# Kernel optimization log

Hardware: AMD Instinct MI355X
Metric: run time of the kernel (lower is better)

The kernel has to match this reference:

```python
import jax, jax.numpy as jnp
import numpy as np

B, S, D = 2, 2048, 1024
H, KV, HD = 16, 4, 64
E, TOPK, F = 8, 2, 2048
EPS = 1e-5
THETA = 10000.0


def setup_inputs() -> dict:
    key = jax.random.key(0)
    ks = jax.random.split(key, 12)
    sc = 0.02
    x = jax.random.normal(ks[0], (B, S, D), jnp.float32)
    # real RoPE tables
    inv = 1.0 / (THETA ** (np.arange(0, HD, 2, dtype=np.float32) / HD))
    t = np.arange(S, dtype=np.float32)
    f = np.outer(t, inv)  # [S, HD/2]
    freqs_cos = jnp.asarray(np.cos(f), jnp.float32)
    freqs_sin = jnp.asarray(np.sin(f), jnp.float32)
    return {
        "x": x,
        "freqs_cos": freqs_cos,
        "freqs_sin": freqs_sin,
        "attn_norm_w": jnp.ones((D,), jnp.float32),
        "ffn_norm_w": jnp.ones((D,), jnp.float32),
        "wq": jax.random.normal(ks[1], (D, H * HD), jnp.float32) * sc,
        "wk": jax.random.normal(ks[2], (D, KV * HD), jnp.float32) * sc,
        "wv": jax.random.normal(ks[3], (D, KV * HD), jnp.float32) * sc,
        "wo": jax.random.normal(ks[4], (H * HD, D), jnp.float32) * sc,
        "gate_w": jax.random.normal(ks[5], (D, E), jnp.float32) * sc,
        "w1": jax.random.normal(ks[6], (E, D, F), jnp.float32) * sc,
        "w2": jax.random.normal(ks[7], (E, F, D), jnp.float32) * sc,
        "w3": jax.random.normal(ks[8], (E, D, F), jnp.float32) * sc,
    }


def rmsnorm(x, w):
    return x * jax.lax.rsqrt(jnp.mean(x * x, axis=-1, keepdims=True) + EPS) * w


def apply_rope(xq, cos, sin):
    # xq: [B,S,h,HD]; cos/sin: [S, HD/2]
    xr, xi = xq[..., 0::2], xq[..., 1::2]
    c = cos[None, :, None, :]
    s = sin[None, :, None, :]
    out = jnp.stack([xr * c - xi * s, xr * s + xi * c], axis=-1)
    return out.reshape(xq.shape)


def attention(xn, freqs_cos, freqs_sin, wq, wk, wv, wo):
    q = (xn @ wq).reshape(B, S, H, HD)
    k = (xn @ wk).reshape(B, S, KV, HD)
    v = (xn @ wv).reshape(B, S, KV, HD)
    q = apply_rope(q, freqs_cos, freqs_sin)
    k = apply_rope(k, freqs_cos, freqs_sin)
    n_rep = H // KV
    k = jnp.repeat(k, n_rep, axis=2)  # [B,S,H,HD]
    v = jnp.repeat(v, n_rep, axis=2)
    scores = jnp.einsum("bqhd,bkhd->bhqk", q, k) / jnp.sqrt(jnp.float32(HD))
    causal = jnp.tril(jnp.ones((S, S), bool))
    scores = jnp.where(causal[None, None], scores, jnp.finfo(scores.dtype).min)
    probs = jax.nn.softmax(scores, axis=-1)
    out = jnp.einsum("bhqk,bkhd->bqhd", probs, v).reshape(B, S, H * HD)
    return out @ wo


def sparse_moe(hn, gate_w, w1, w2, w3):
    xf = hn.reshape(-1, D)  # [T, D]
    probs = jax.nn.softmax(xf @ gate_w, axis=-1)  # [T, E]
    topv, topi = jax.lax.top_k(probs, TOPK)
    topv = topv / jnp.sum(topv, axis=-1, keepdims=True)
    # dense [T, E] routing weights (0 for non-selected experts)
    wdense = jnp.sum(jax.nn.one_hot(topi, E, dtype=xf.dtype) * topv[..., None], axis=1)
    h1 = jax.nn.silu(jnp.einsum("td,edf->etf", xf, w1))
    h3 = jnp.einsum("td,edf->etf", xf, w3)
    y = jnp.einsum("etf,efd->etd", h1 * h3, w2)
    out = jnp.einsum("te,etd->td", wdense, y)
    return out.reshape(B, S, D)


def reference(x, freqs_cos, freqs_sin, attn_norm_w, ffn_norm_w,
              wq, wk, wv, wo, gate_w, w1, w2, w3):
    h = x + attention(rmsnorm(x, attn_norm_w), freqs_cos, freqs_sin, wq, wk, wv, wo)
    out = h + sparse_moe(rmsnorm(h, ffn_norm_w), gate_w, w1, w2, w3)
    return out
```

## Files before the change

### kernel.cpp

```cpp
#include <hip/hip_runtime.h>
#include <stdint.h>

typedef unsigned short u16;
typedef unsigned int u32;
typedef __attribute__((ext_vector_type(8))) short short8;
typedef __attribute__((ext_vector_type(8))) u16 us8;
typedef __attribute__((ext_vector_type(4))) u16 us4;
typedef __attribute__((ext_vector_type(4))) float f32x4;

constexpr int NB = 2;
constexpr int SEQ = 2048;
constexpr int DIM = 1024;
constexpr int NH = 16;
constexpr int HD = 64;
constexpr int NE = 8;
constexpr int FF = 2048;
constexpr int TOK = NB * SEQ;
constexpr int NQKV = 1536;
constexpr int NPAIR = TOK * 2;
constexpr float REPS = 1e-5f;

__device__ __forceinline__ u16 f2bf(float x) {
  union { float f; u32 u; } v; v.f = x;
  u32 r = v.u + 0x7fffu + ((v.u >> 16) & 1u);
  return (u16)(r >> 16);
}
__device__ __forceinline__ float bf2f(u16 h) {
  union { u32 u; float f; } v; v.u = ((u32)h) << 16;
  return v.f;
}

__device__ __forceinline__ void gl_lds16(const u16* g, u16* l) {
  __builtin_amdgcn_global_load_lds(
      (const __attribute__((address_space(1))) void*)g,
      (__attribute__((address_space(3))) void*)l, 16, 0, 0);
}

template <bool SPLIT>
__global__ __launch_bounds__(256) void tcvt_k(const float* __restrict__ src,
                                              u16* __restrict__ dhi,
                                              u16* __restrict__ dlo,
                                              int K, int N) {
  int z = blockIdx.z;
  src += (size_t)z * K * N;
  dhi += (size_t)z * K * N;
  if (SPLIT) dlo += (size_t)z * K * N;
  int n0 = blockIdx.x * 64, k0 = blockIdx.y * 64;
  __shared__ float tile[64][65];
  int t = threadIdx.x;
  int kk = t >> 4, nn4 = (t & 15) * 4;
#pragma unroll
  for (int i = 0; i < 4; i++) {
    int k = kk + i * 16;
    const float* p = src + (size_t)(k0 + k) * N + n0 + nn4;
    float4 v = *(const float4*)p;
    tile[nn4 + 0][k] = v.x;
    tile[nn4 + 1][k] = v.y;
    tile[nn4 + 2][k] = v.z;
    tile[nn4 + 3][k] = v.w;
  }
  __syncthreads();
  int nn = t >> 4, k4 = (t & 15) * 4;
#pragma unroll
  for (int i = 0; i < 4; i++) {
    int n = nn + i * 16;
    us4 hi, lo;
#pragma unroll
    for (int j = 0; j < 4; j++) {
      float f = tile[n][k4 + j];
      u16 h = f2bf(f);
      hi[j] = h;
      if (SPLIT) lo[j] = f2bf(f - bf2f(h));
    }
    *(us4*)(dhi + (size_t)(n0 + n) * K + k0 + k4) = hi;
    if (SPLIT) *(us4*)(dlo + (size_t)(n0 + n) * K + k0 + k4) = lo;
  }
}

template <bool SPLIT>
__global__ __launch_bounds__(256) void rmsnorm_k(const float* __restrict__ x,
                                                 const float* __restrict__ w,
                                                 u16* __restrict__ ohi,
                                                 u16* __restrict__ olo) {
  int row = blockIdx.x, t = threadIdx.x;
  float4 v = *(const float4*)(x + (size_t)row * DIM + t * 4);
  float ss = v.x * v.x + v.y * v.y + v.z * v.z + v.w * v.w;
#pragma unroll
  for (int m = 1; m < 64; m <<= 1) ss += __shfl_xor(ss, m);
  __shared__ float red[4];
  if ((t & 63) == 0) red[t >> 6] = ss;
  __syncthreads();
  float rstd = rsqrtf((red[0] + red[1] + red[2] + red[3]) * (1.0f / DIM) + REPS);
  float4 wv = *(const float4*)(w + t * 4);
  float os[4] = {v.x * rstd * wv.x, v.y * rstd * wv.y, v.z * rstd * wv.z,
                 v.w * rstd * wv.w};
  us4 hi, lo;
#pragma unroll
  for (int j = 0; j < 4; j++) {
    u16 h = f2bf(os[j]);
    hi[j] = h;
    if (SPLIT) lo[j] = f2bf(os[j] - bf2f(h));
  }
  *(us4*)(ohi + (size_t)row * DIM + t * 4) = hi;
  if (SPLIT) *(us4*)(olo + (size_t)row * DIM + t * 4) = lo;
}

template <int EPI, bool SPLIT, bool DUAL, bool PERSIST, bool GATHER, int NXL,
          int NT, int BN>
__global__ __launch_bounds__(256, 2) void gemm_k(
    const u16* __restrict__ Ah, const u16* __restrict__ Al,
    const u16* __restrict__ Bh, const u16* __restrict__ Bl,
    const u16* __restrict__ Bd, int N, int ldc,
    float* __restrict__ Cf, u16* __restrict__ Cb, float* __restrict__ C2,
    const float* __restrict__ resid, const int* __restrict__ cnt,
    const int* __restrict__ pids, const float* __restrict__ pw,
    const int* __restrict__ plan) {
  constexpr int K = NT * 64;
  constexpr int WCOL = BN / 2;
  constexpr int FN = BN / 32;

  int tid = threadIdx.x, lane = tid & 63, wid = tid >> 6;
  int wm = wid >> 1, wn = wid & 1;
  int rr = lane & 15, g = lane >> 4;

  __shared__ u16 sAh[128 * 64];
  __shared__ u16 sAl[SPLIT ? 128 * 64 : 16];
  __shared__ u16 sBh[BN * 64];
  __shared__ u16 sBl[SPLIT ? BN * 64 : 16];
  __shared__ u16 sB1[DUAL ? BN * 64 : 16];
  __shared__ int spid[PERSIST ? 128 : 8];
  __shared__ int srow[GATHER ? 128 : 8];

  int pl[9];
  int items;
  if (PERSIST) {
#pragma unroll
    for (int e = 0; e < 9; e++) pl[e] = plan[e];
    items = pl[8] << NXL;
  } else {
    items = 1;
  }

  int it0, itstep;
  if (PERSIST) {
    int nb = gridDim.x;
    it0 = ((nb & 7) == 0) ? ((blockIdx.x & 7) * (nb >> 3) + (blockIdx.x >> 3))
                          : blockIdx.x;
    itstep = nb;
  } else {
    it0 = 0;
    itstep = 1;
  }
  for (int w = it0; w < items; w += itstep) {
    int m0, n0, z, yt, cntz;
    if (PERSIST) {
      int wy = w >> NXL;
      int x = w & ((1 << NXL) - 1);
      z = 0;
#pragma unroll
      for (int e = 1; e < 8; e++) z += (wy >= pl[e]) ? 1 : 0;
      yt = wy - pl[z];
      m0 = wy * 128;
      n0 = x * BN;
      cntz = cnt[z];
      __syncthreads();
      if (tid < 128) {
        int i = yt * 128 + tid;
        if (i > cntz - 1) i = cntz - 1;
        int p = pids[z * NPAIR + i];
        spid[tid] = p;
        if (GATHER) srow[tid] = p >> 1;
      }
      __syncthreads();
    } else {
      int gx = gridDim.x;
      int nb = gx * gridDim.y;
      int lin = blockIdx.y * gx + blockIdx.x;
      int v = ((nb & 7) == 0) ? ((lin & 7) * (nb >> 3) + (lin >> 3)) : lin;
      m0 = (v / gx) * 128;
      n0 = (v % gx) * BN;
      z = 0;
      yt = 0;
      cntz = 1 << 30;
    }

    const u16* Bhz = Bh + (size_t)z * N * K;
    const u16* Blz = SPLIT ? Bl + (size_t)z * N * K : nullptr;
    const u16* Bdz = DUAL ? Bd + (size_t)z * N * K : nullptr;

    const u16 *agh[4], *agl[SPLIT ? 4 : 1];
    int aoff[4];
#pragma unroll
    for (int i = 0; i < 4; i++) {
      int cid = tid + i * 256;
      int r = cid >> 3, c = cid & 7;
      int gr = GATHER ? srow[r] : (m0 + r);
      int sc = c ^ (r & 7);
      agh[i] = Ah + (size_t)gr * K + sc * 8;
      if (SPLIT) agl[i] = Al + (size_t)gr * K + sc * 8;
      aoff[i] = r * 64 + c * 8;
    }
    const u16 *bgh[FN], *bgl[SPLIT ? FN : 1], *bg1[DUAL ? FN : 1];
    int boff[FN];
#pragma unroll
    for (int i = 0; i < FN; i++) {
      int cid = tid + i * 256;
      int r = cid >> 3, c = cid & 7;
      int sc = c ^ (r & 7);
      size_t gr = (size_t)(n0 + r) * K + sc * 8;
      bgh[i] = Bhz + gr;
      if (SPLIT) bgl[i] = Blz + gr;
      if (DUAL) bg1[i] = Bdz + gr;
      boff[i] = r * 64 + c * 8;
    }

    f32x4 zv = {0.f, 0.f, 0.f, 0.f};
    f32x4 acc[4][FN];
    f32x4 acc1[DUAL ? 4 : 1][DUAL ? FN : 1];
#pragma unroll
    for (int a = 0; a < 4; a++)
#pragma unroll
      for (int b = 0; b < FN; b++) {
        acc[a][b] = zv;
        if (DUAL) acc1[a][b] = zv;
      }

    for (int t = 0; t < NT; t++) {
      int k0 = t * 64;
      __syncthreads();
#pragma unroll
      for (int i = 0; i < 4; i++) {
        gl_lds16(agh[i] + k0, sAh + aoff[i]);
        if (SPLIT) gl_lds16(agl[i] + k0, sAl + aoff[i]);
      }
#pragma unroll
      for (int i = 0; i < FN; i++) {
        gl_lds16(bgh[i] + k0, sBh + boff[i]);
        if (SPLIT) gl_lds16(bgl[i] + k0, sBl + boff[i]);
        if (DUAL) gl_lds16(bg1[i] + k0, sB1 + boff[i]);
      }
      __syncthreads();

#pragma unroll
      for (int kc = 0; kc < 2; kc++) {
        short8 a_h[4], a_l[SPLIT ? 4 : 1], b_h[FN], b_l[SPLIT ? FN : 1],
            b1f[DUAL ? FN : 1];
#pragma unroll
        for (int f = 0; f < 4; f++) {
          int ra = wm * 64 + f * 16 + rr;
          int off = ra * 64 + (((kc * 4 + g) ^ (ra & 7)) * 8);
          a_h[f] = *(const short8*)&sAh[off];
          if (SPLIT) a_l[f] = *(const short8*)&sAl[off];
        }
#pragma unroll
        for (int f = 0; f < FN; f++) {
          int rb = wn * WCOL + f * 16 + rr;
          int off = rb * 64 + (((kc * 4 + g) ^ (rb & 7)) * 8);
          b_h[f] = *(const short8*)&sBh[off];
          if (SPLIT) b_l[f] = *(const short8*)&sBl[off];
          if (DUAL) b1f[f] = *(const short8*)&sB1[off];
        }
#pragma unroll
        for (int fm = 0; fm < 4; fm++)
#pragma unroll
          for (int fn = 0; fn < FN; fn++) {
            acc[fm][fn] = __builtin_amdgcn_mfma_f32_16x16x32_bf16(
                a_h[fm], b_h[fn], acc[fm][fn], 0, 0, 0);
            if (SPLIT) {
              acc[fm][fn] = __builtin_amdgcn_mfma_f32_16x16x32_bf16(
                  a_h[fm], b_l[fn], acc[fm][fn], 0, 0, 0);
              acc[fm][fn] = __builtin_amdgcn_mfma_f32_16x16x32_bf16(
                  a_l[fm], b_h[fn], acc[fm][fn], 0, 0, 0);
            }
            if (DUAL)
              acc1[fm][fn] = __builtin_amdgcn_mfma_f32_16x16x32_bf16(
                  a_h[fm], b1f[fn], acc1[fm][fn], 0, 0, 0);
          }
      }
    }

#pragma unroll
    for (int fm = 0; fm < 4; fm++)
#pragma unroll
      for (int fn = 0; fn < FN; fn++)
#pragma unroll
        for (int rg = 0; rg < 4; rg++) {
          int rl = wm * 64 + fm * 16 + g * 4 + rg;
          int col = n0 + wn * WCOL + fn * 16 + rr;
          float v = acc[fm][fn][rg];
          if (EPI == 0) {
            Cf[(size_t)(m0 + rl) * ldc + col] = v;
          } else if (EPI == 1) {
            size_t idx = (size_t)(m0 + rl) * ldc + col;
            float r2 = v + resid[idx];
            Cf[idx] = r2;
            C2[idx] = r2;
          } else if (EPI == 2) {
            float gg = v / (1.0f + __expf(-v));
            float o = gg * acc1[fm][fn][rg];
            Cb[(size_t)(m0 + rl) * ldc + col] = f2bf(o);
          } else {
            int i = yt * 128 + rl;
            if (i < cntz) {
              int p = spid[rl];
              atomicAdd(&Cf[(size_t)(p >> 1) * ldc + col], pw[p] * v);
            }
          }
        }
  }
}

__global__ __launch_bounds__(256) void rope_k(float* __restrict__ qkv,
                                              const float* __restrict__ fc,
                                              const float* __restrict__ fs) {
  int idx = blockIdx.x * 256 + threadIdx.x;
  int i = idx & 31;
  int hh = (idx >> 5) % 20;
  int t = idx / 640;
  if (t >= TOK) return;
  int s = t & (SEQ - 1);
  int base = (hh < 16) ? (hh * 64) : (1024 + (hh - 16) * 64);
  float c = fc[s * 32 + i], sn = fs[s * 32 + i];
  float* p = qkv + (size_t)t * NQKV + base + 2 * i;
  float xr = p[0], xi = p[1];
  p[0] = xr * c - xi * sn;
  p[1] = xr * sn + xi * c;
}

__global__ __launch_bounds__(256) void cvtkv_k(const float* __restrict__ qkv,
                                               u16* __restrict__ Kh,
                                               u16* __restrict__ Kl,
                                               u16* __restrict__ Vh,
                                               u16* __restrict__ Vl) {
  int kvt = blockIdx.x;
  int kvh = blockIdx.y;
  int b = blockIdx.z;
  int t = threadIdx.x;
  __shared__ float vt[64][65];
  size_t tile = ((size_t)((b * 4 + kvh) * 32 + kvt)) * 4096;
  int r = t >> 2, c4 = t & 3;
  {
    const float* kp = qkv + ((size_t)(b * SEQ + kvt * 64 + r)) * NQKV + 1024 +
                      kvh * 64 + c4 * 16;
    float ff[16];
#pragma unroll
    for (int q = 0; q < 4; q++) {
      float4 f = *(const float4*)(kp + q * 4);
      ff[q * 4 + 0] = f.x; ff[q * 4 + 1] = f.y;
      ff[q * 4 + 2] = f.z; ff[q * 4 + 3] = f.w;
    }
#pragma unroll
    for (int half = 0; half < 2; half++) {
      int c = c4 * 2 + half;
      us8 hi, lo;
#pragma unroll
      for (int j = 0; j < 8; j++) {
        float f = ff[half * 8 + j];
        u16 h = f2bf(f);
        hi[j] = h;
        lo[j] = f2bf(f - bf2f(h));
      }
      int off = r * 64 + ((c ^ (r & 7)) * 8);
      *(us8*)(Kh + tile + off) = hi;
      *(us8*)(Kl + tile + off) = lo;
    }
  }
  {
    const float* vp = qkv + ((size_t)(b * SEQ + kvt * 64 + r)) * NQKV + 1280 +
                      kvh * 64 + c4 * 16;
#pragma unroll
    for (int q = 0; q < 4; q++) {
      float4 f = *(const float4*)(vp + q * 4);
      vt[r][c4 * 16 + q * 4 + 0] = f.x;
      vt[r][c4 * 16 + q * 4 + 1] = f.y;
      vt[r][c4 * 16 + q * 4 + 2] = f.z;
      vt[r][c4 * 16 + q * 4 + 3] = f.w;
    }
  }
  __syncthreads();
  {
    int d = t >> 2, g4 = t & 3;
    float ff[16];
#pragma unroll
    for (int j = 0; j < 16; j++) ff[j] = vt[g4 * 16 + j][d];
#pragma unroll
    for (int half = 0; half < 2; half++) {
      int c = g4 * 2 + half;
      us8 hi, lo;
#pragma unroll
      for (int j = 0; j < 8; j++) {
        float f = ff[half * 8 + j];
        u16 h = f2bf(f);
        hi[j] = h;
        lo[j] = f2bf(f - bf2f(h));
      }
      int off = d * 64 + ((c ^ (d & 7)) * 8);
      *(us8*)(Vh + tile + off) = hi;
      *(us8*)(Vl + tile + off) = lo;
    }
  }
}

__global__ __launch_bounds__(256, 2) void flash_k(
    const float* __restrict__ qkv, const u16* __restrict__ Kg,
    const u16* __restrict__ Klg, const u16* __restrict__ Vg,
    const u16* __restrict__ Vlg, u16* __restrict__ ah, u16* __restrict__ al) {
  int pi = blockIdx.x;
  int h = blockIdx.y;
  int b = blockIdx.z;
  int qt[2] = {31 - pi, pi};
  int kvh = h >> 2;
  int tid = threadIdx.x, lane = tid & 63, wid = tid >> 6;
  int rr = lane & 15, g = lane >> 4;

  __shared__ u16 sKh[4096], sKl[4096], sVh[4096], sVl[4096];
  __shared__ u32 sP[4][1024];

  f32x4 zv = {0.f, 0.f, 0.f, 0.f};
  short8 aqh[2][2], aql[2][2];
#pragma unroll
  for (int u = 0; u < 2; u++) {
    int qrow = qt[u] * 64 + wid * 16 + rr;
    const float* qp =
        qkv + ((size_t)(b * SEQ + qrow)) * NQKV + h * 64 + g * 8;
#pragma unroll
    for (int kc = 0; kc < 2; kc++) {
      float4 f0 = *(const float4*)(qp + kc * 32);
      float4 f1 = *(const float4*)(qp + kc * 32 + 4);
      float ff[8] = {f0.x, f0.y, f0.z, f0.w, f1.x, f1.y, f1.z, f1.w};
#pragma unroll
      for (int j = 0; j < 8; j++) {
        u16 hi = f2bf(ff[j]);
        aqh[u][kc][j] = (short)hi;
        aql[u][kc][j] = (short)f2bf(ff[j] - bf2f(hi));
      }
    }
  }

  f32x4 o[2][4];
  float m_r[2][4], l_r[2][4];
#pragma unroll
  for (int u = 0; u < 2; u++)
#pragma unroll
    for (int i = 0; i < 4; i++) {
      o[u][i] = zv;
      m_r[u][i] = -3.0e38f;
      l_r[u][i] = 0.f;
    }

  size_t tb = ((size_t)(b * 4 + kvh) * 32) * 4096;
  int so = tid * 16;
  us8 rKh[2], rKl[2], rVh[2], rVl[2];
  {
    size_t go = tb + so;
    rKh[0] = *(const us8*)(Kg + go);  rKh[1] = *(const us8*)(Kg + go + 8);
    rKl[0] = *(const us8*)(Klg + go); rKl[1] = *(const us8*)(Klg + go + 8);
    rVh[0] = *(const us8*)(Vg + go);  rVh[1] = *(const us8*)(Vg + go + 8);
    rVl[0] = *(const us8*)(Vlg + go); rVl[1] = *(const us8*)(Vlg + go + 8);
  }

  int nt = qt[0];
  for (int kvt = 0; kvt <= nt; kvt++) {
    __syncthreads();
    *(us8*)&sKh[so] = rKh[0]; *(us8*)&sKh[so + 8] = rKh[1];
    *(us8*)&sKl[so] = rKl[0]; *(us8*)&sKl[so + 8] = rKl[1];
    *(us8*)&sVh[so] = rVh[0]; *(us8*)&sVh[so + 8] = rVh[1];
    *(us8*)&sVl[so] = rVl[0]; *(us8*)&sVl[so + 8] = rVl[1];
    if (kvt < nt) {
      size_t go = tb + (size_t)(kvt + 1) * 4096 + so;
      rKh[0] = *(const us8*)(Kg + go);  rKh[1] = *(const us8*)(Kg + go + 8);
      rKl[0] = *(const us8*)(Klg + go); rKl[1] = *(const us8*)(Klg + go + 8);
      rVh[0] = *(const us8*)(Vg + go);  rVh[1] = *(const us8*)(Vg + go + 8);
      rVl[0] = *(const us8*)(Vlg + go); rVl[1] = *(const us8*)(Vlg + go + 8);
    }
    __syncthreads();

#pragma unroll
    for (int u = 0; u < 2; u++) {
      if (!(u == 1 && kvt > qt[1])) {
        float pv[4][4];
#pragma unroll
        for (int c16 = 0; c16 < 4; c16++) {
          int rk = c16 * 16 + rr;
          f32x4 sacc = zv;
#pragma unroll
          for (int kc = 0; kc < 2; kc++) {
            int sw = rk * 64 + (((kc * 4 + g) ^ (rk & 7)) * 8);
            short8 bh = *(const short8*)&sKh[sw];
            short8 bl = *(const short8*)&sKl[sw];
            sacc = __builtin_amdgcn_mfma_f32_16x16x32_bf16(aqh[u][kc], bh,
                                                           sacc, 0, 0, 0);
            sacc = __builtin_amdgcn_mfma_f32_16x16x32_bf16(aqh[u][kc], bl,
                                                           sacc, 0, 0, 0);
            sacc = __builtin_amdgcn_mfma_f32_16x16x32_bf16(aql[u][kc], bh,
                                                           sacc, 0, 0, 0);
          }
          bool diag = (kvt == qt[u]);
#pragma unroll
          for (int rg = 0; rg < 4; rg++) {
            float val = sacc[rg] * 0.125f;
            if (diag) {
              int kv_l = c16 * 16 + rr;
              int q_l = wid * 16 + g * 4 + rg;
              if (kv_l > q_l) val = -3.0e38f;
            }
            pv[c16][rg] = val;
          }
        }
        float pm[4];
#pragma unroll
        for (int rg = 0; rg < 4; rg++)
          pm[rg] = fmaxf(fmaxf(pv[0][rg], pv[1][rg]),
                         fmaxf(pv[2][rg], pv[3][rg]));
#pragma unroll
        for (int m = 1; m < 16; m <<= 1)
#pragma unroll
          for (int rg = 0; rg < 4; rg++)
            pm[rg] = fmaxf(pm[rg], __shfl_xor(pm[rg], m));
        float scl[4];
#pragma unroll
        for (int rg = 0; rg < 4; rg++) {
          float mn = fmaxf(m_r[u][rg], pm[rg]);
          scl[rg] = __expf(m_r[u][rg] - mn);
          m_r[u][rg] = mn;
        }
#pragma unroll
        for (int c16 = 0; c16 < 4; c16++)
#pragma unroll
          for (int rg = 0; rg < 4; rg++)
            pv[c16][rg] = __expf(pv[c16][rg] - m_r[u][rg]);
        float rsum[4];
#pragma unroll
        for (int rg = 0; rg < 4; rg++)
          rsum[rg] = pv[0][rg] + pv[1][rg] + pv[2][rg] + pv[3][rg];
#pragma unroll
        for (int m = 1; m < 16; m <<= 1)
#pragma unroll
          for (int rg = 0; rg < 4; rg++) rsum[rg] += __shfl_xor(rsum[rg], m);
#pragma unroll
        for (int rg = 0; rg < 4; rg++)
          l_r[u][rg] = l_r[u][rg] * scl[rg] + rsum[rg];
#pragma unroll
        for (int d16 = 0; d16 < 4; d16++)
#pragma unroll
          for (int rg = 0; rg < 4; rg++) o[u][d16][rg] *= scl[rg];

#pragma unroll
        for (int c16 = 0; c16 < 4; c16++)
#pragma unroll
          for (int rg = 0; rg < 4; rg++) {
            int ql = g * 4 + rg;
            int kvl = c16 * 16 + rr;
            u16 hi = f2bf(pv[c16][rg]);
            u16 lo = f2bf(pv[c16][rg] - bf2f(hi));
            sP[wid][ql * 64 + (kvl ^ (((ql >> 2) & 3) << 4))] =
                ((u32)lo << 16) | (u32)hi;
          }
        short8 pah[2], pal[2];
#pragma unroll
        for (int kc = 0; kc < 2; kc++) {
          int xb = (kc * 32 + g * 8) ^ (((rr >> 2) & 3) << 4);
          const u32* pp = &sP[wid][rr * 64 + xb];
#pragma unroll
          for (int j = 0; j < 8; j++) {
            u32 w = pp[j];
            pah[kc][j] = (short)(w & 0xffffu);
            pal[kc][j] = (short)(w >> 16);
          }
        }
#pragma unroll
        for (int d16 = 0; d16 < 4; d16++) {
          int rv = d16 * 16 + rr;
#pragma unroll
          for (int kc = 0; kc < 2; kc++) {
            int sw = rv * 64 + (((kc * 4 + g) ^ (rv & 7)) * 8);
            short8 vh = *(const short8*)&sVh[sw];
            short8 vl = *(const short8*)&sVl[sw];
            o[u][d16] = __builtin_amdgcn_mfma_f32_16x16x32_bf16(
                pah[kc], vh, o[u][d16], 0, 0, 0);
            o[u][d16] = __builtin_amdgcn_mfma_f32_16x16x32_bf16(
                pah[kc], vl, o[u][d16], 0, 0, 0);
            o[u][d16] = __builtin_amdgcn_mfma_f32_16x16x32_bf16(
                pal[kc], vh, o[u][d16], 0, 0, 0);
          }
        }
      }
    }
  }

#pragma unroll
  for (int u = 0; u < 2; u++)
#pragma unroll
    for (int rg = 0; rg < 4; rg++) {
      float inv = 1.0f / l_r[u][rg];
      int qr = qt[u] * 64 + wid * 16 + g * 4 + rg;
      size_t obase = (size_t)(b * SEQ + qr) * 1024 + h * 64;
#pragma unroll
      for (int d16 = 0; d16 < 4; d16++) {
        float v = o[u][d16][rg] * inv;
        u16 hi = f2bf(v);
        ah[obase + d16 * 16 + rr] = hi;
        al[obase + d16 * 16 + rr] = f2bf(v - bf2f(hi));
      }
    }
}

__global__ __launch_bounds__(256) void route_k(const float* __restrict__ h,
                                               const float* __restrict__ wffn,
                                               const float* __restrict__ gw,
                                               int* __restrict__ cnt,
                                               int* __restrict__ pids,
                                               float* __restrict__ pw) {
  int t = blockIdx.x, tid = threadIdx.x;
  float4 v = *(const float4*)(h + (size_t)t * DIM + tid * 4);
  float ss = v.x * v.x + v.y * v.y + v.z * v.z + v.w * v.w;
#pragma unroll
  for (int m = 1; m < 64; m <<= 1) ss += __shfl_xor(ss, m);
  __shared__ float red[4];
  if ((tid & 63) == 0) red[tid >> 6] = ss;
  __syncthreads();
  float rstd = rsqrtf((red[0] + red[1] + red[2] + red[3]) * (1.0f / DIM) + REPS);
  float4 wv = *(const float4*)(wffn + tid * 4);
  float xn[4] = {v.x * rstd * wv.x, v.y * rstd * wv.y, v.z * rstd * wv.z,
                 v.w * rstd * wv.w};
  float pl[8] = {0, 0, 0, 0, 0, 0, 0, 0};
#pragma unroll
  for (int j = 0; j < 4; j++) {
    const float* gp = gw + (size_t)(tid * 4 + j) * 8;
    float4 g0 = *(const float4*)gp;
    float4 g1 = *(const float4*)(gp + 4);
    pl[0] += xn[j] * g0.x; pl[1] += xn[j] * g0.y;
    pl[2] += xn[j] * g0.z; pl[3] += xn[j] * g0.w;
    pl[4] += xn[j] * g1.x; pl[5] += xn[j] * g1.y;
    pl[6] += xn[j] * g1.z; pl[7] += xn[j] * g1.w;
  }
#pragma unroll
  for (int e = 0; e < 8; e++)
#pragma unroll
    for (int m = 1; m < 64; m <<= 1) pl[e] += __shfl_xor(pl[e], m);
  __shared__ float lred[4][8];
  if ((tid & 63) == 0)
#pragma unroll
    for (int e = 0; e < 8; e++) lred[tid >> 6][e] = pl[e];
  __syncthreads();
  if (tid == 0) {
    float lg[8];
#pragma unroll
    for (int e = 0; e < 8; e++)
      lg[e] = lred[0][e] + lred[1][e] + lred[2][e] + lred[3][e];
    int e1 = 0;
    float l1 = lg[0];
#pragma unroll
    for (int e = 1; e < 8; e++)
      if (lg[e] > l1) { l1 = lg[e]; e1 = e; }
    int e2 = -1;
    float l2 = -3.0e38f;
#pragma unroll
    for (int e = 0; e < 8; e++)
      if (e != e1 && lg[e] > l2) { l2 = lg[e]; e2 = e; }
    float w1 = 1.0f / (1.0f + expf(l2 - l1));
    float w2 = 1.0f / (1.0f + expf(l1 - l2));
    int p0 = atomicAdd(&cnt[e1], 1);
    pids[e1 * NPAIR + p0] = t * 2;
    pw[t * 2] = w1;
    int p1 = atomicAdd(&cnt[e2], 1);
    pids[e2 * NPAIR + p1] = t * 2 + 1;
    pw[t * 2 + 1] = w2;
  }
}

__global__ void zero_k(int* cnt) {
  if (threadIdx.x < 8) cnt[threadIdx.x] = 0;
}

__global__ void plan_k(const int* __restrict__ cnt, int* __restrict__ plan) {
  if (threadIdx.x == 0) {
    int acc = 0;
    for (int e = 0; e < 8; e++) {
      plan[e] = acc;
      acc += (cnt[e] + 127) >> 7;
    }
    plan[8] = acc;
  }
}

extern "C" void kernel_launch(void* const* d_in, const int* in_sizes, int n_in,
                              void* d_out, int out_size, void* d_ws,
                              size_t ws_size, hipStream_t stream) {
  (void)in_sizes; (void)n_in; (void)out_size; (void)ws_size;
  const float* x = (const float*)d_in[0];
  const float* fc = (const float*)d_in[1];
  const float* fs = (const float*)d_in[2];
  const float* anw = (const float*)d_in[3];
  const float* fnw = (const float*)d_in[4];
  const float* wq = (const float*)d_in[5];
  const float* wk = (const float*)d_in[6];
  const float* wv = (const float*)d_in[7];
  const float* wo = (const float*)d_in[8];
  const float* gw = (const float*)d_in[9];
  const float* w1 = (const float*)d_in[10];
  const float* w2 = (const float*)d_in[11];
  const float* w3 = (const float*)d_in[12];
  float* outf = (float*)d_out;

  char* ws = (char*)d_ws;
  size_t off = 0;
  auto alloc = [&](size_t bytes) {
    void* p = ws + off;
    off += (bytes + 255) & ~(size_t)255;
    return p;
  };
  u16* xnh = (u16*)alloc((size_t)TOK * DIM * 2);
  u16* xnl = (u16*)alloc((size_t)TOK * DIM * 2);
  float* qkvf = (float*)alloc((size_t)TOK * NQKV * 4);
  u16* h13 = xnh;
  u16* wqkvT_h = (u16*)alloc((size_t)NQKV * DIM * 2);
  u16* wqkvT_l = (u16*)alloc((size_t)NQKV * DIM * 2);
  u16* woT_h = (u16*)alloc((size_t)DIM * DIM * 2);
  u16* woT_l = (u16*)alloc((size_t)DIM * DIM * 2);
  u16* w1T = (u16*)alloc((size_t)NE * FF * DIM * 2);
  u16* w3T = (u16*)alloc((size_t)NE * FF * DIM * 2);
  u16* w2T = (u16*)alloc((size_t)NE * DIM * FF * 2);
  u16* attnh = (u16*)alloc((size_t)TOK * DIM * 2);
  u16* attnl = (u16*)alloc((size_t)TOK * DIM * 2);
  float* hbuf = (float*)alloc((size_t)TOK * DIM * 4);
  u16* hn = (u16*)alloc((size_t)TOK * DIM * 2);
  int* cnt = (int*)alloc(64);
  int* plan = (int*)alloc(64);
  int* pids = (int*)alloc((size_t)NE * NPAIR * 4);
  float* pwbuf = (float*)alloc((size_t)NPAIR * 4);
  u16* Ksw_h = (u16*)alloc((size_t)NB * 4 * SEQ * 64 * 2);
  u16* Ksw_l = (u16*)alloc((size_t)NB * 4 * SEQ * 64 * 2);
  u16* Vsw_h = (u16*)alloc((size_t)NB * 4 * SEQ * 64 * 2);
  u16* Vsw_l = (u16*)alloc((size_t)NB * 4 * SEQ * 64 * 2);

  dim3 blk(256);
  hipLaunchKernelGGL((tcvt_k<true>), dim3(16, 16, 1), blk, 0, stream, wq,
                     wqkvT_h, wqkvT_l, 1024, 1024);
  hipLaunchKernelGGL((tcvt_k<true>), dim3(4, 16, 1), blk, 0, stream, wk,
                     wqkvT_h + 1024 * 1024, wqkvT_l + 1024 * 1024, 1024, 256);
  hipLaunchKernelGGL((tcvt_k<true>), dim3(4, 16, 1), blk, 0, stream, wv,
                     wqkvT_h + 1280 * 1024, wqkvT_l + 1280 * 1024, 1024, 256);
  hipLaunchKernelGGL((tcvt_k<true>), dim3(16, 16, 1), blk, 0, stream, wo, woT_h,
                     woT_l, 1024, 1024);
  hipLaunchKernelGGL((tcvt_k<false>), dim3(32, 16, 8), blk, 0, stream, w1, w1T,
                     (u16*)nullptr, 1024, 2048);
  hipLaunchKernelGGL((tcvt_k<false>), dim3(32, 16, 8), blk, 0, stream, w3, w3T,
                     (u16*)nullptr, 1024, 2048);
  hipLaunchKernelGGL((tcvt_k<false>), dim3(16, 32, 8), blk, 0, stream, w2, w2T,
                     (u16*)nullptr, 2048, 1024);
  hipLaunchKernelGGL((rmsnorm_k<true>), dim3(TOK), blk, 0, stream, x, anw, xnh,
                     xnl);
  hipLaunchKernelGGL((gemm_k<0, true, false, false, false, 0, 16, 64>),
                     dim3(NQKV / 64, TOK / 128, 1), blk, 0, stream, xnh, xnl,
                     wqkvT_h, wqkvT_l, (const u16*)nullptr, NQKV, NQKV, qkvf,
                     (u16*)nullptr, (float*)nullptr, (const float*)nullptr,
                     (const int*)nullptr, (const int*)nullptr,
                     (const float*)nullptr, (const int*)nullptr);
  hipLaunchKernelGGL(rope_k, dim3((TOK * 20 * 32) / 256), blk, 0, stream, qkvf,
                     fc, fs);
  hipLaunchKernelGGL(cvtkv_k, dim3(SEQ / 64, 4, NB), blk, 0, stream, qkvf,
                     Ksw_h, Ksw_l, Vsw_h, Vsw_l);
  hipLaunchKernelGGL(flash_k, dim3(16, NH, NB), blk, 0, stream, qkvf, Ksw_h,
                     Ksw_l, Vsw_h, Vsw_l, attnh, attnl);
  hipLaunchKernelGGL((gemm_k<1, true, false, false, false, 0, 16, 64>),
                     dim3(DIM / 64, TOK / 128, 1), blk, 0, stream, attnh, attnl,
                     woT_h, woT_l, (const u16*)nullptr, DIM, DIM, hbuf,
                     (u16*)nullptr, outf, x, (const int*)nullptr,
                     (const int*)nullptr, (const float*)nullptr,
                     (const int*)nullptr);
  hipLaunchKernelGGL((rmsnorm_k<false>), dim3(TOK), blk, 0, stream, hbuf, fnw,
                     hn, (u16*)nullptr);
  hipLaunchKernelGGL(zero_k, dim3(1), dim3(64), 0, stream, cnt);
  hipLaunchKernelGGL(route_k, dim3(TOK), blk, 0, stream, hbuf, fnw, gw, cnt,
                     pids, pwbuf);
  hipLaunchKernelGGL(plan_k, dim3(1), dim3(64), 0, stream, cnt, plan);
  hipLaunchKernelGGL((gemm_k<2, false, true, true, true, 4, 16, 128>),
                     dim3(512), blk, 0, stream, hn, (const u16*)nullptr, w1T,
                     (const u16*)nullptr, w3T, FF, FF, (float*)nullptr, h13,
                     (float*)nullptr, (const float*)nullptr, cnt, pids, pwbuf,
                     plan);
  hipLaunchKernelGGL((gemm_k<3, false, false, true, false, 3, 32, 128>),
                     dim3(512), blk, 0, stream, h13, (const u16*)nullptr, w2T,
                     (const u16*)nullptr, (const u16*)nullptr, DIM, DIM, outf,
                     (u16*)nullptr, (float*)nullptr, (const float*)nullptr, cnt,
                     pids, pwbuf, plan);
}
```

Baseline: 580.5 us.

## Add split-K to expert down-projection GEMM and raise occupancy bounds

Adds a split-K template parameter to the GEMM kernel so the expert w2 GEMM (K=2048) is split into two K-halves processed by separate work items. This relies on the EPI 3 epilogue accumulating into the output, presumably atomically. It also raises the launch_bounds minimum waves per EU to 3 or 4 and enlarges the persistent grids, aiming for more latency hiding and better load balance. The risks are register pressure or spills from the tighter bounds, and extra atomic or accumulation traffic from the split-K partials.

```diff
diff --git a/kernel.cpp b/kernel.cpp
--- a/kernel.cpp
+++ b/kernel.cpp
@@ -106,8 +106,8 @@
 }
 
 template <int EPI, bool SPLIT, bool DUAL, bool PERSIST, bool GATHER, int NXL,
-          int NT, int BN>
-__global__ __launch_bounds__(256, 2) void gemm_k(
+          int NT, int BN, int NKS, int MINW>
+__global__ __launch_bounds__(256, MINW) void gemm_k(
     const u16* __restrict__ Ah, const u16* __restrict__ Al,
     const u16* __restrict__ Bh, const u16* __restrict__ Bl,
     const u16* __restrict__ Bd, int N, int ldc,
@@ -116,6 +116,7 @@
     const int* __restrict__ pids, const float* __restrict__ pw,
     const int* __restrict__ plan) {
   constexpr int K = NT * 64;
+  constexpr int KT = K * NKS;
   constexpr int WCOL = BN / 2;
   constexpr int FN = BN / 32;
 
@@ -152,10 +153,12 @@
     itstep = 1;
   }
   for (int w = it0; w < items; w += itstep) {
-    int m0, n0, z, yt, cntz;
+    int m0, n0, z, yt, cntz, ks;
     if (PERSIST) {
       int wy = w >> NXL;
-      int x = w & ((1 << NXL) - 1);
+      int sub = w & ((1 << NXL) - 1);
+      int x = sub / NKS;
+      ks = sub % NKS;
       z = 0;
 #pragma unroll
       for (int e = 1; e < 8; e++) z += (wy >= pl[e]) ? 1 : 0;
@@ -182,11 +185,13 @@
       z = 0;
       yt = 0;
       cntz = 1 << 30;
-    }
-
-    const u16* Bhz = Bh + (size_t)z * N * K;
-    const u16* Blz = SPLIT ? Bl + (size_t)z * N * K : nullptr;
-    const u16* Bdz = DUAL ? Bd + (size_t)z * N * K : nullptr;
+      ks = 0;
+    }
+
+    const u16* Bhz = Bh + (size_t)z * N * KT;
+    const u16* Blz = SPLIT ? Bl + (size_t)z * N * KT : nullptr;
+    const u16* Bdz = DUAL ? Bd + (size_t)z * N * KT : nullptr;
+    int kbase = ks * K;
 
     const u16 *agh[4], *agl[SPLIT ? 4 : 1];
     int aoff[4];
@@ -196,8 +201,8 @@
       int r = cid >> 3, c = cid & 7;
       int gr = GATHER ? srow[r] : (m0 + r);
       int sc = c ^ (r & 7);
-      agh[i] = Ah + (size_t)gr * K + sc * 8;
-      if (SPLIT) agl[i] = Al + (size_t)gr * K + sc * 8;
+      agh[i] = Ah + (size_t)gr * KT + kbase + sc * 8;
+      if (SPLIT) agl[i] = Al + (size_t)gr * KT + kbase + sc * 8;
       aoff[i] = r * 64 + c * 8;
     }
     const u16 *bgh[FN], *bgl[SPLIT ? FN : 1], *bg1[DUAL ? FN : 1];
@@ -207,7 +212,7 @@
       int cid = tid + i * 256;
       int r = cid >> 3, c = cid & 7;
       int sc = c ^ (r & 7);
-      size_t gr = (size_t)(n0 + r) * K + sc * 8;
+      size_t gr = (size_t)(n0 + r) * KT + kbase + sc * 8;
       bgh[i] = Bhz + gr;
       if (SPLIT) bgl[i] = Blz + gr;
       if (DUAL) bg1[i] = Bdz + gr;
@@ -751,7 +756,7 @@
                      (u16*)nullptr, 2048, 1024);
   hipLaunchKernelGGL((rmsnorm_k<true>), dim3(TOK), blk, 0, stream, x, anw, xnh,
                      xnl);
-  hipLaunchKernelGGL((gemm_k<0, true, false, false, false, 0, 16, 64>),
+  hipLaunchKernelGGL((gemm_k<0, true, false, false, false, 0, 16, 64, 1, 3>),
                      dim3(NQKV / 64, TOK / 128, 1), blk, 0, stream, xnh, xnl,
                      wqkvT_h, wqkvT_l, (const u16*)nullptr, NQKV, NQKV, qkvf,
                      (u16*)nullptr, (float*)nullptr, (const float*)nullptr,
@@ -763,7 +768,7 @@
                      Ksw_h, Ksw_l, Vsw_h, Vsw_l);
   hipLaunchKernelGGL(flash_k, dim3(16, NH, NB), blk, 0, stream, qkvf, Ksw_h,
                      Ksw_l, Vsw_h, Vsw_l, attnh, attnl);
-  hipLaunchKernelGGL((gemm_k<1, true, false, false, false, 0, 16, 64>),
+  hipLaunchKernelGGL((gemm_k<1, true, false, false, false, 0, 16, 64, 1, 3>),
                      dim3(DIM / 64, TOK / 128, 1), blk, 0, stream, attnh, attnl,
                      woT_h, woT_l, (const u16*)nullptr, DIM, DIM, hbuf,
                      (u16*)nullptr, outf, x, (const int*)nullptr,
@@ -775,13 +780,13 @@
   hipLaunchKernelGGL(route_k, dim3(TOK), blk, 0, stream, hbuf, fnw, gw, cnt,
                      pids, pwbuf);
   hipLaunchKernelGGL(plan_k, dim3(1), dim3(64), 0, stream, cnt, plan);
-  hipLaunchKernelGGL((gemm_k<2, false, true, true, true, 4, 16, 128>),
-                     dim3(512), blk, 0, stream, hn, (const u16*)nullptr, w1T,
+  hipLaunchKernelGGL((gemm_k<2, false, true, true, true, 4, 16, 128, 1, 3>),
+                     dim3(1024), blk, 0, stream, hn, (const u16*)nullptr, w1T,
                      (const u16*)nullptr, w3T, FF, FF, (float*)nullptr, h13,
                      (float*)nullptr, (const float*)nullptr, cnt, pids, pwbuf,
                      plan);
-  hipLaunchKernelGGL((gemm_k<3, false, false, true, false, 3, 32, 128>),
-                     dim3(512), blk, 0, stream, h13, (const u16*)nullptr, w2T,
+  hipLaunchKernelGGL((gemm_k<3, false, false, true, false, 4, 16, 128, 2, 4>),
+                     dim3(1152), blk, 0, stream, h13, (const u16*)nullptr, w2T,
                      (const u16*)nullptr, (const u16*)nullptr, DIM, DIM, outf,
                      (u16*)nullptr, (float*)nullptr, (const float*)nullptr, cnt,
                      pids, pwbuf, plan);
```

After: 707.8 us. +21.9%, slower.
